# Kernel optimization log

Measured on AMD Instinct MI355X. Metric: run time of the kernel, lower is better.

The kernel has to match this reference:

```python
import jax, jax.numpy as jnp
import numpy as np

D_MODEL = 1024
N_HEADS = 16
D_HEAD = D_MODEL // N_HEADS
HIDDEN = 4096
B, T = 2, 2048
EPS = 1e-5


def setup_inputs() -> dict:
    key = jax.random.key(0)
    ks = jax.random.split(key, 16)
    s = 0.02
    return {
        "x": jax.random.normal(ks[0], (B, T, D_MODEL), dtype=jnp.float32),
        # LayerNorm 1
        "gamma1": jnp.ones((D_MODEL,), jnp.float32),
        "beta1": jnp.zeros((D_MODEL,), jnp.float32),
        # attention projections, stored (in, out) so y = x @ W + b
        "Wq": jax.random.normal(ks[1], (D_MODEL, D_MODEL), jnp.float32) * s,
        "bq": jnp.zeros((D_MODEL,), jnp.float32),
        "Wk": jax.random.normal(ks[2], (D_MODEL, D_MODEL), jnp.float32) * s,
        "bk": jnp.zeros((D_MODEL,), jnp.float32),
        "Wv": jax.random.normal(ks[3], (D_MODEL, D_MODEL), jnp.float32) * s,
        "bv": jnp.zeros((D_MODEL,), jnp.float32),
        "Wo": jax.random.normal(ks[4], (D_MODEL, D_MODEL), jnp.float32) * s,
        "bo": jnp.zeros((D_MODEL,), jnp.float32),
        # LayerNorm 2
        "gamma2": jnp.ones((D_MODEL,), jnp.float32),
        "beta2": jnp.zeros((D_MODEL,), jnp.float32),
        # MLP
        "W1": jax.random.normal(ks[5], (D_MODEL, HIDDEN), jnp.float32) * s,
        "b1": jnp.zeros((HIDDEN,), jnp.float32),
        "W2": jax.random.normal(ks[6], (HIDDEN, D_MODEL), jnp.float32) * s,
        "b2": jnp.zeros((D_MODEL,), jnp.float32),
    }


def _layernorm(x, gamma, beta):
    mean = jnp.mean(x, axis=-1, keepdims=True)
    var = jnp.mean(jnp.square(x - mean), axis=-1, keepdims=True)  # unbiased=False
    return gamma * (x - mean) * jax.lax.rsqrt(var + EPS) + beta


def _attention(x, Wq, bq, Wk, bk, Wv, bv, Wo, bo):
    b, t, _ = x.shape
    q = (x @ Wq + bq).reshape(b, t, N_HEADS, D_HEAD)
    k = (x @ Wk + bk).reshape(b, t, N_HEADS, D_HEAD)
    v = (x @ Wv + bv).reshape(b, t, N_HEADS, D_HEAD)
    scores = jnp.einsum("bqhd,bkhd->bhqk", q, k) / np.sqrt(D_HEAD).astype(np.float32)
    causal = jnp.tril(jnp.ones((t, t), dtype=bool))  # keep j <= i
    scores = jnp.where(causal, scores, -jnp.inf)
    attn = jax.nn.softmax(scores, axis=-1)
    out = jnp.einsum("bhqk,bkhd->bqhd", attn, v).reshape(b, t, D_MODEL)
    return out @ Wo + bo


def reference(x, gamma1, beta1, Wq, bq, Wk, bk, Wv, bv, Wo, bo,
              gamma2, beta2, W1, b1, W2, b2):
    # x = x + Attn(LN1(x))
    x = x + _attention(_layernorm(x, gamma1, beta1), Wq, bq, Wk, bk, Wv, bv, Wo, bo)
    # x = x + MLP(LN2(x)); torch F.gelu default = exact erf gelu
    h = _layernorm(x, gamma2, beta2)
    h = jax.nn.gelu(h @ W1 + b1, approximate=False) @ W2 + b2
    return x + h
```

## Files before the change

kernel.cpp:

```cpp
#include <hip/hip_runtime.h>
#include <stdint.h>

typedef unsigned short u16;
typedef short bf16x8 __attribute__((ext_vector_type(8)));
typedef float f32x4 __attribute__((ext_vector_type(4)));
typedef float f32x16 __attribute__((ext_vector_type(16)));

#define MB (1024L*1024L)

__device__ inline u16 f2bf(float f) {
  union { float f; unsigned u; } v; v.f = f;
  unsigned r = (v.u + 0x7FFFu + ((v.u >> 16) & 1u)) >> 16;
  return (u16)r;
}

__device__ inline float bf2f(u16 u) {
  union { unsigned u; float f; } v; v.u = ((unsigned)u) << 16; return v.f;
}

__device__ inline unsigned cvtpk(float lo, float hi) {
  unsigned r;
  asm("v_cvt_pk_bf16_f32 %0, %1, %2" : "=v"(r) : "v"(lo), "v"(hi));
  return r;
}

#define GLOAD16(gptr, lptr) \
  __builtin_amdgcn_global_load_lds((__attribute__((address_space(1))) void*)(gptr), \
                                   (__attribute__((address_space(3))) void*)(lptr), 16, 0, 0)

__global__ __launch_bounds__(256) void twconv(const float* __restrict__ W,
                                              u16* __restrict__ WT, int K, int N) {
  __shared__ float tile[32][33];
  const int nbn = N >> 5;
  const int bk = blockIdx.x / nbn;
  const int bn = blockIdx.x % nbn;
  const int tid = threadIdx.x;
  const int r = tid >> 3;
  const int c4 = (tid & 7) << 2;
  const float4 v = *(const float4*)(W + (size_t)(bk * 32 + r) * N + bn * 32 + c4);
  tile[r][c4 + 0] = v.x; tile[r][c4 + 1] = v.y;
  tile[r][c4 + 2] = v.z; tile[r][c4 + 3] = v.w;
  __syncthreads();
  ushort4 o;
  o.x = f2bf(tile[c4 + 0][r]); o.y = f2bf(tile[c4 + 1][r]);
  o.z = f2bf(tile[c4 + 2][r]); o.w = f2bf(tile[c4 + 3][r]);
  *(ushort4*)(WT + (size_t)(bn * 32 + r) * K + bk * 32 + c4) = o;
}

__global__ __launch_bounds__(256) void concat3(const float* __restrict__ a,
                                               const float* __restrict__ b,
                                               const float* __restrict__ c,
                                               float* __restrict__ out, int n) {
  int i = blockIdx.x * 256 + threadIdx.x;
  if (i < n) { out[i] = a[i]; out[n + i] = b[i]; out[2 * n + i] = c[i]; }
}

__global__ __launch_bounds__(256) void ln_kernel(const float* __restrict__ x,
                                                 const float* __restrict__ gamma,
                                                 const float* __restrict__ beta,
                                                 u16* __restrict__ out) {
  const int row = blockIdx.x;
  const int tid = threadIdx.x;
  const float4 v = *(const float4*)(x + (size_t)row * 1024 + tid * 4);
  float s = v.x + v.y + v.z + v.w;
  float s2 = v.x * v.x + v.y * v.y + v.z * v.z + v.w * v.w;
#pragma unroll
  for (int m = 1; m < 64; m <<= 1) {
    s += __shfl_xor(s, m, 64);
    s2 += __shfl_xor(s2, m, 64);
  }
  __shared__ float red[8];
  const int w = tid >> 6;
  if ((tid & 63) == 0) { red[w] = s; red[4 + w] = s2; }
  __syncthreads();
  s = red[0] + red[1] + red[2] + red[3];
  s2 = red[4] + red[5] + red[6] + red[7];
  const float mean = s * (1.0f / 1024.0f);
  const float var = s2 * (1.0f / 1024.0f) - mean * mean;
  const float rstd = rsqrtf(var + 1e-5f);
  const float4 g = *(const float4*)(gamma + tid * 4);
  const float4 b = *(const float4*)(beta + tid * 4);
  ushort4 o;
  o.x = f2bf(g.x * (v.x - mean) * rstd + b.x);
  o.y = f2bf(g.y * (v.y - mean) * rstd + b.y);
  o.z = f2bf(g.z * (v.z - mean) * rstd + b.z);
  o.w = f2bf(g.w * (v.w - mean) * rstd + b.w);
  *(ushort4*)(out + (size_t)row * 1024 + tid * 4) = o;
}

template <int EPI, int BN>
__global__ __launch_bounds__(256, (BN == 64) ? 3 : 2)
void gemm_bt(const u16* __restrict__ A, const u16* __restrict__ BT,
             const float* __restrict__ bias, const float* __restrict__ res,
             void* __restrict__ outp, int M, int N, int K) {
  constexpr int MF = (BN == 128) ? 4 : 2;
  constexpr int ACH = 4;
  constexpr int BCH = BN / 32;
  constexpr int LOADS = ACH + BCH;
  __shared__ __align__(16) u16 As[2][128 * 64];
  __shared__ __align__(16) u16 Bs[2][BN * 64];
  const int nBN = N / BN;
  const int hw = blockIdx.x;
  const int xcd = hw & 7;
  const int rr = hw >> 3;
  const int bm = xcd * 4 + rr / nBN;
  const int bn = rr % nBN;
  const int tid = threadIdx.x;
  const int lane = tid & 63;
  const int wid = tid >> 6;
  const int wm = (BN == 128) ? (wid >> 1) : wid;
  const int wn = (BN == 128) ? (wid & 1) : 0;
  const int e4 = lane >> 4;

  int abase[MF], ax[MF];
#pragma unroll
  for (int m = 0; m < MF; ++m) {
    int rowa = wm * (MF * 16) + m * 16 + (lane & 15);
    abase[m] = rowa * 64; ax[m] = rowa & 7;
  }
  int bbase[4], bx[4];
#pragma unroll
  for (int n = 0; n < 4; ++n) {
    int rowb = wn * 64 + n * 16 + (lane & 15);
    bbase[n] = rowb * 64; bx[n] = rowb & 7;
  }

  size_t ga[ACH]; int loa[ACH];
#pragma unroll
  for (int c = 0; c < ACH; ++c) {
    int idx = tid + (c << 8);
    int row = idx >> 3;
    int ch = (idx & 7) ^ (row & 7);
    ga[c] = (size_t)(bm * 128 + row) * K + (ch << 3);
    loa[c] = idx << 4;
  }
  size_t gb[BCH]; int lob[BCH];
#pragma unroll
  for (int c = 0; c < BCH; ++c) {
    int idx = tid + (c << 8);
    int row = idx >> 3;
    int ch = (idx & 7) ^ (row & 7);
    gb[c] = (size_t)(bn * BN + row) * K + (ch << 3);
    lob[c] = idx << 4;
  }

#define STAGE_G(t, bb) do { \
  _Pragma("unroll") for (int c = 0; c < ACH; ++c) \
    GLOAD16(A + ga[c] + (size_t)(t) * 64, (char*)As[bb] + loa[c]); \
  _Pragma("unroll") for (int c = 0; c < BCH; ++c) \
    GLOAD16(BT + gb[c] + (size_t)(t) * 64, (char*)Bs[bb] + lob[c]); \
} while (0)

  f32x4 acc[MF][4] = {};
  const int nt = K >> 6;

  STAGE_G(0, 0);
  STAGE_G(1, 1);

  for (int t = 0; t < nt; ++t) {
    if (t + 1 < nt) {
      asm volatile("s_waitcnt vmcnt(%0)" :: "i"(LOADS) : "memory");
    } else {
      asm volatile("s_waitcnt vmcnt(0)" ::: "memory");
    }
    __builtin_amdgcn_s_barrier();
    const u16* Ap = As[t & 1];
    const u16* Bp = Bs[t & 1];
    bf16x8 af[2][MF], bfr[2][4];
#pragma unroll
    for (int kk = 0; kk < 2; ++kk) {
#pragma unroll
      for (int m = 0; m < MF; ++m)
        af[kk][m] = *(const bf16x8*)(Ap + abase[m] + (((((kk << 2) | e4)) ^ ax[m]) << 3));
#pragma unroll
      for (int n = 0; n < 4; ++n)
        bfr[kk][n] = *(const bf16x8*)(Bp + bbase[n] + (((((kk << 2) | e4)) ^ bx[n]) << 3));
    }
    asm volatile("s_waitcnt lgkmcnt(0)" ::: "memory");
    __builtin_amdgcn_s_barrier();
    if (t + 2 < nt) STAGE_G(t + 2, t & 1);
    __builtin_amdgcn_s_setprio(1);
#pragma unroll
    for (int kk = 0; kk < 2; ++kk)
#pragma unroll
      for (int m = 0; m < MF; ++m)
#pragma unroll
        for (int n = 0; n < 4; ++n)
          acc[m][n] = __builtin_amdgcn_mfma_f32_16x16x32_bf16(af[kk][m], bfr[kk][n], acc[m][n], 0, 0, 0);
    __builtin_amdgcn_s_setprio(0);
  }
#undef STAGE_G

  const int rbase = bm * 128 + wm * (MF * 16);
  const int cbase = bn * BN + wn * 64;
#pragma unroll
  for (int m = 0; m < MF; ++m) {
#pragma unroll
    for (int n = 0; n < 4; ++n) {
      const int col = cbase + n * 16 + (lane & 15);
      const int row0 = rbase + m * 16 + ((lane >> 4) << 2);
      const float bv = bias[col];
#pragma unroll
      for (int r = 0; r < 4; ++r) {
        const int row = row0 + r;
        float v = acc[m][n][r] + bv;
        if (EPI == 1) {
          ((float*)outp)[(size_t)row * N + col] = v + res[(size_t)row * N + col];
        } else if (EPI == 2) {
          float tt = v * (1.0f + 0.044715f * v * v);
          float sg = 1.0f / (1.0f + __expf(-1.5957691216057308f * tt));
          ((u16*)outp)[(size_t)row * N + col] = f2bf(v * sg);
        } else {
          ((u16*)outp)[(size_t)row * N + col] = f2bf(v);
        }
      }
    }
  }
}

__global__ __launch_bounds__(512, 2) void attn_kernel(const u16* __restrict__ QKV,
                                                      u16* __restrict__ O) {
  __shared__ __align__(16) u16 KV[4][4096];
  const int T = 2048, LD = 3072;
  const int blk = blockIdx.x;
  const int xcd = blk & 7;
  const int i = blk >> 3;
  const int bh = xcd * 4 + (i & 3);
  const int p = i >> 2;
  const int b = bh >> 4, hd = bh & 15;
  const int tid = threadIdx.x;
  const int lane = tid & 63;
  const int w = tid >> 6;
  const int h = lane >> 5;
  const int cA = p, cB = 15 - p;
  const int myc = (w < 4) ? cA : cB;
  const int qwb = myc * 128 + (w & 3) * 32;
  const int qg = qwb + (lane & 31);
  const int diag = qwb >> 6;
  const int myNt = diag + 1;
  const int nt = 2 * cB + 2;

  const u16* Qb = QKV + (size_t)b * T * LD + hd * 64;
  const u16* Kb = Qb + 1024;
  const u16* Vb = Qb + 2048;

  const float QSC = 0.18033688011112042f;
  bf16x8 qf[4];
#pragma unroll
  for (int s = 0; s < 4; ++s) {
    bf16x8 raw = *(const bf16x8*)(Qb + (size_t)qg * LD + s * 16 + h * 8);
    union { unsigned wd[4]; bf16x8 v; } u;
#pragma unroll
    for (int e = 0; e < 4; ++e)
      u.wd[e] = cvtpk(bf2f((u16)raw[2 * e]) * QSC, bf2f((u16)raw[2 * e + 1]) * QSC);
    qf[s] = u.v;
  }

  f32x16 oacc[2] = {};
  float m = -INFINITY, l = 0.0f;

  const int srow = tid >> 3;
  const int scol = tid & 7;
  const int kgc = ((scol ^ (srow & 7)) << 3);

  GLOAD16(Kb + (size_t)srow * LD + kgc, (char*)KV[0] + tid * 16);
  {
    bf16x8 vv0 = *(const bf16x8*)(Vb + (size_t)srow * LD + scol * 8);
#pragma unroll
    for (int e = 0; e < 8; ++e) {
      int d = scol * 8 + e;
      KV[2][(d << 6) | (srow & 7) | ((((srow >> 3) ^ e ^ scol) & 7) << 3)] = (u16)vv0[e];
    }
  }
  __syncthreads();

  int cur = 0;
  for (int j = 0; j < nt; ++j) {
    const bool pre = (j + 1 < nt);
    bf16x8 vv;
    if (pre) {
      GLOAD16(Kb + (size_t)((j + 1) * 64 + srow) * LD + kgc, (char*)KV[cur ^ 1] + tid * 16);
      vv = *(const bf16x8*)(Vb + (size_t)((j + 1) * 64 + srow) * LD + scol * 8);
    }

    if (j < myNt) {
      f32x16 sacc[2] = {};
      const u16* Kp = KV[cur];
      __builtin_amdgcn_s_setprio(1);
#pragma unroll
      for (int t = 0; t < 2; ++t) {
#pragma unroll
        for (int s = 0; s < 4; ++s) {
          int row = t * 32 + (lane & 31);
          bf16x8 kf = *(const bf16x8*)(Kp + (row << 6) + ((((2 * s + h) ^ (row & 7)) & 7) << 3));
          sacc[t] = __builtin_amdgcn_mfma_f32_32x32x16_bf16(kf, qf[s], sacc[t], 0, 0, 0);
        }
      }
      __builtin_amdgcn_s_setprio(0);

      if (j == diag) {
#pragma unroll
        for (int t = 0; t < 2; ++t)
#pragma unroll
          for (int r = 0; r < 16; ++r) {
            int key = (j << 6) + 32 * t + (r & 3) + 8 * (r >> 2) + 4 * h;
            if (key > qg) sacc[t][r] = -INFINITY;
          }
      }

      float pmax = -INFINITY;
#pragma unroll
      for (int t = 0; t < 2; ++t)
#pragma unroll
        for (int r = 0; r < 16; ++r) pmax = fmaxf(pmax, sacc[t][r]);
      pmax = fmaxf(pmax, __shfl_xor(pmax, 32, 64));

      if (!__all(pmax - m <= 2.8853900817779268f)) {
        float mn = fmaxf(m, pmax);
        float alpha = exp2f(m - mn);
        m = mn;
        l *= alpha;
#pragma unroll
        for (int d2 = 0; d2 < 2; ++d2)
#pragma unroll
          for (int r = 0; r < 16; ++r) oacc[d2][r] *= alpha;
      }

      float lsum = 0.0f;
#pragma unroll
      for (int t = 0; t < 2; ++t)
#pragma unroll
        for (int r = 0; r < 16; ++r) {
          float pe = exp2f(sacc[t][r] - m);
          sacc[t][r] = pe;
          lsum += pe;
        }
      lsum += __shfl_xor(lsum, 32, 64);
      l += lsum;

      union PF { unsigned wd[4]; bf16x8 v; } pf[4];
#pragma unroll
      for (int t = 0; t < 2; ++t) {
#pragma unroll
        for (int kb = 0; kb < 2; ++kb) {
          int base = 8 * kb;
          unsigned A0 = cvtpk(sacc[t][base + 0], sacc[t][base + 1]);
          unsigned A2 = cvtpk(sacc[t][base + 2], sacc[t][base + 3]);
          unsigned A4 = cvtpk(sacc[t][base + 4], sacc[t][base + 5]);
          unsigned A6 = cvtpk(sacc[t][base + 6], sacc[t][base + 7]);
          unsigned S0 = (unsigned)__shfl_xor((int)(h ? A0 : A4), 32, 64);
          unsigned S2 = (unsigned)__shfl_xor((int)(h ? A2 : A6), 32, 64);
          PF& u = pf[2 * t + kb];
          u.wd[0] = h ? S0 : A0;
          u.wd[1] = h ? S2 : A2;
          u.wd[2] = h ? A4 : S0;
          u.wd[3] = h ? A6 : S2;
        }
      }

      const u16* Vp = KV[2 + cur];
      __builtin_amdgcn_s_setprio(1);
#pragma unroll
      for (int d2 = 0; d2 < 2; ++d2) {
        int d = d2 * 32 + (lane & 31);
#pragma unroll
        for (int ks = 0; ks < 4; ++ks) {
          bf16x8 vf = *(const bf16x8*)(Vp + (d << 6) + ((((2 * ks + h) ^ (d & 7) ^ ((d >> 3) & 7)) & 7) << 3));
          oacc[d2] = __builtin_amdgcn_mfma_f32_32x32x16_bf16(vf, pf[ks].v, oacc[d2], 0, 0, 0);
        }
      }
      __builtin_amdgcn_s_setprio(0);
    }

    if (pre) {
#pragma unroll
      for (int e = 0; e < 8; ++e) {
        int d = scol * 8 + e;
        KV[2 + (cur ^ 1)][(d << 6) | (srow & 7) | ((((srow >> 3) ^ e ^ scol) & 7) << 3)] = (u16)vv[e];
      }
    }
    __syncthreads();
    cur ^= 1;
  }

  const float rinv = 1.0f / l;
  u16* Ob = (u16*)KV;
  const int qloc = w * 32 + (lane & 31);
#pragma unroll
  for (int d2 = 0; d2 < 2; ++d2)
#pragma unroll
    for (int r = 0; r < 16; ++r) {
      int d = d2 * 32 + (r & 3) + 8 * (r >> 2) + 4 * h;
      Ob[(qloc << 6) | (d ^ ((qloc & 7) << 3))] = f2bf(oacc[d2][r] * rinv);
    }
  __syncthreads();
#pragma unroll
  for (int it = 0; it < 4; ++it) {
    int r = (tid >> 3) + it * 64;
    int c = tid & 7;
    bf16x8 val = *(const bf16x8*)(Ob + (r << 6) + (((c ^ (r & 7)) & 7) << 3));
    int qg2 = (r < 128) ? (cA * 128 + r) : (cB * 128 + (r - 128));
    *(bf16x8*)(O + (size_t)(b * T + qg2) * 1024 + hd * 64 + c * 8) = val;
  }
}

extern "C" void kernel_launch(void* const* d_in, const int* in_sizes, int n_in,
                              void* d_out, int out_size, void* d_ws, size_t ws_size,
                              hipStream_t stream) {
  const float* x      = (const float*)d_in[0];
  const float* gamma1 = (const float*)d_in[1];
  const float* beta1  = (const float*)d_in[2];
  const float* Wq     = (const float*)d_in[3];
  const float* bq     = (const float*)d_in[4];
  const float* Wk     = (const float*)d_in[5];
  const float* bk     = (const float*)d_in[6];
  const float* Wv     = (const float*)d_in[7];
  const float* bv     = (const float*)d_in[8];
  const float* Wo     = (const float*)d_in[9];
  const float* bo     = (const float*)d_in[10];
  const float* gamma2 = (const float*)d_in[11];
  const float* beta2  = (const float*)d_in[12];
  const float* W1     = (const float*)d_in[13];
  const float* b1     = (const float*)d_in[14];
  const float* W2     = (const float*)d_in[15];
  const float* b2     = (const float*)d_in[16];

  char* ws = (char*)d_ws;
  u16* WqkvT = (u16*)(ws + 0 * MB);
  u16* WoT   = (u16*)(ws + 6 * MB);
  u16* W1T   = (u16*)(ws + 8 * MB);
  u16* W2T   = (u16*)(ws + 16 * MB);
  u16* qkv   = (u16*)(ws + 24 * MB);
  u16* hb    = (u16*)(ws + 24 * MB);
  u16* xn    = (u16*)(ws + 56 * MB);
  float* bqkv = (float*)d_out;
  float* x1 = (float*)d_out;

  const int M = 4096;

  twconv<<<dim3(1024), dim3(256), 0, stream>>>(Wq, WqkvT, 1024, 1024);
  twconv<<<dim3(1024), dim3(256), 0, stream>>>(Wk, WqkvT + 1024 * 1024, 1024, 1024);
  twconv<<<dim3(1024), dim3(256), 0, stream>>>(Wv, WqkvT + 2048 * 1024, 1024, 1024);
  twconv<<<dim3(1024), dim3(256), 0, stream>>>(Wo, WoT, 1024, 1024);
  twconv<<<dim3(4096), dim3(256), 0, stream>>>(W1, W1T, 1024, 4096);
  twconv<<<dim3(4096), dim3(256), 0, stream>>>(W2, W2T, 4096, 1024);
  concat3<<<dim3(4), dim3(256), 0, stream>>>(bq, bk, bv, bqkv, 1024);

  ln_kernel<<<dim3(M), dim3(256), 0, stream>>>(x, gamma1, beta1, xn);

  gemm_bt<0, 128><<<dim3(768), dim3(256), 0, stream>>>(xn, WqkvT, bqkv, nullptr, qkv, M, 3072, 1024);

  attn_kernel<<<dim3(256), dim3(512), 0, stream>>>(qkv, xn);

  gemm_bt<1, 64><<<dim3(512), dim3(256), 0, stream>>>(xn, WoT, bo, x, x1, M, 1024, 1024);

  ln_kernel<<<dim3(M), dim3(256), 0, stream>>>(x1, gamma2, beta2, xn);

  gemm_bt<2, 128><<<dim3(1024), dim3(256), 0, stream>>>(xn, W1T, b1, nullptr, hb, M, 4096, 1024);
  gemm_bt<1, 64><<<dim3(512), dim3(256), 0, stream>>>(hb, W2T, b2, x1, d_out, M, 1024, 4096);
}
```

Before: 238.6 us.

## Software-pipeline attention: overlap QK of next tile with PV of previous

The attention loop now defers each tile's P·V MFMA work by one iteration. The QK^T MFMAs for tile j and the PV MFMAs for tile j-1 are issued back to back in one high-priority region, and the softmax exp work can overlap with outstanding matrix ops. V staging moves from double to triple buffering, which raises LDS from four to five 8KB slabs. A drain step after the loop handles the last tile. This is meant to hide the softmax dependency latency between QK and PV, at the cost of more LDS and more live registers (sacc and pf are now carried across iterations).

```diff
diff --git a/kernel.cpp b/kernel.cpp
--- a/kernel.cpp
+++ b/kernel.cpp
@@ -220,7 +220,7 @@
 
 __global__ __launch_bounds__(512, 2) void attn_kernel(const u16* __restrict__ QKV,
                                                       u16* __restrict__ O) {
-  __shared__ __align__(16) u16 KV[4][4096];
+  __shared__ __align__(16) u16 SM[5][4096];
   const int T = 2048, LD = 3072;
   const int blk = blockIdx.x;
   const int xcd = blk & 7;
@@ -257,38 +257,46 @@
   }
 
   f32x16 oacc[2] = {};
+  f32x16 sacc[2];
+  union PF { unsigned wd[4]; bf16x8 v; } pf[4];
   float m = -INFINITY, l = 0.0f;
 
   const int srow = tid >> 3;
   const int scol = tid & 7;
   const int kgc = ((scol ^ (srow & 7)) << 3);
 
-  GLOAD16(Kb + (size_t)srow * LD + kgc, (char*)KV[0] + tid * 16);
+#define VWRITE(buf, vvreg) do { \
+  _Pragma("unroll") for (int e = 0; e < 8; ++e) { \
+    int d = scol * 8 + e; \
+    SM[2 + (buf)][(d << 6) | (srow & 7) | ((((srow >> 3) ^ e ^ scol) & 7) << 3)] = (u16)(vvreg)[e]; \
+  } \
+} while (0)
+
+  GLOAD16(Kb + (size_t)srow * LD + kgc, (char*)SM[0] + tid * 16);
   {
     bf16x8 vv0 = *(const bf16x8*)(Vb + (size_t)srow * LD + scol * 8);
-#pragma unroll
-    for (int e = 0; e < 8; ++e) {
-      int d = scol * 8 + e;
-      KV[2][(d << 6) | (srow & 7) | ((((srow >> 3) ^ e ^ scol) & 7) << 3)] = (u16)vv0[e];
-    }
+    VWRITE(0, vv0);
   }
   __syncthreads();
 
-  int cur = 0;
+  int vPrev = 2, vCur = 0, vNext = 1;
   for (int j = 0; j < nt; ++j) {
     const bool pre = (j + 1 < nt);
     bf16x8 vv;
     if (pre) {
-      GLOAD16(Kb + (size_t)((j + 1) * 64 + srow) * LD + kgc, (char*)KV[cur ^ 1] + tid * 16);
+      GLOAD16(Kb + (size_t)((j + 1) * 64 + srow) * LD + kgc, (char*)SM[(j + 1) & 1] + tid * 16);
       vv = *(const bf16x8*)(Vb + (size_t)((j + 1) * 64 + srow) * LD + scol * 8);
     }
-
-    if (j < myNt) {
-      f32x16 sacc[2] = {};
-      const u16* Kp = KV[cur];
-      __builtin_amdgcn_s_setprio(1);
+    const bool doQK = (j < myNt);
+    const bool doPV = (j >= 1) && (j <= myNt);
+
+    __builtin_amdgcn_s_setprio(1);
+    if (doQK) {
+      const u16* Kp = SM[j & 1];
 #pragma unroll
       for (int t = 0; t < 2; ++t) {
+#pragma unroll
+        for (int r = 0; r < 16; ++r) sacc[t][r] = 0.0f;
 #pragma unroll
         for (int s = 0; s < 4; ++s) {
           int row = t * 32 + (lane & 31);
@@ -296,8 +304,22 @@
           sacc[t] = __builtin_amdgcn_mfma_f32_32x32x16_bf16(kf, qf[s], sacc[t], 0, 0, 0);
         }
       }
-      __builtin_amdgcn_s_setprio(0);
-
+    }
+    if (doPV) {
+      const u16* Vp = SM[2 + vPrev];
+#pragma unroll
+      for (int d2 = 0; d2 < 2; ++d2) {
+        int d = d2 * 32 + (lane & 31);
+#pragma unroll
+        for (int ks = 0; ks < 4; ++ks) {
+          bf16x8 vf = *(const bf16x8*)(Vp + (d << 6) + ((((2 * ks + h) ^ (d & 7) ^ ((d >> 3) & 7)) & 7) << 3));
+          oacc[d2] = __builtin_amdgcn_mfma_f32_32x32x16_bf16(vf, pf[ks].v, oacc[d2], 0, 0, 0);
+        }
+      }
+    }
+    __builtin_amdgcn_s_setprio(0);
+
+    if (doQK) {
       if (j == diag) {
 #pragma unroll
         for (int t = 0; t < 2; ++t)
@@ -338,7 +360,6 @@
       lsum += __shfl_xor(lsum, 32, 64);
       l += lsum;
 
-      union PF { unsigned wd[4]; bf16x8 v; } pf[4];
 #pragma unroll
       for (int t = 0; t < 2; ++t) {
 #pragma unroll
@@ -357,34 +378,29 @@
           u.wd[3] = h ? A6 : S2;
         }
       }
-
-      const u16* Vp = KV[2 + cur];
-      __builtin_amdgcn_s_setprio(1);
-#pragma unroll
-      for (int d2 = 0; d2 < 2; ++d2) {
-        int d = d2 * 32 + (lane & 31);
-#pragma unroll
-        for (int ks = 0; ks < 4; ++ks) {
-          bf16x8 vf = *(const bf16x8*)(Vp + (d << 6) + ((((2 * ks + h) ^ (d & 7) ^ ((d >> 3) & 7)) & 7) << 3));
-          oacc[d2] = __builtin_amdgcn_mfma_f32_32x32x16_bf16(vf, pf[ks].v, oacc[d2], 0, 0, 0);
-        }
-      }
-      __builtin_amdgcn_s_setprio(0);
-    }
-
-    if (pre) {
-#pragma unroll
-      for (int e = 0; e < 8; ++e) {
-        int d = scol * 8 + e;
-        KV[2 + (cur ^ 1)][(d << 6) | (srow & 7) | ((((srow >> 3) ^ e ^ scol) & 7) << 3)] = (u16)vv[e];
-      }
-    }
+    }
+
+    if (pre) VWRITE(vNext, vv);
     __syncthreads();
-    cur ^= 1;
-  }
+    vPrev = vCur; vCur = vNext; vNext = (vNext == 2) ? 0 : (vNext + 1);
+  }
+
+  if (myNt == nt) {
+    const u16* Vp = SM[2 + vPrev];
+#pragma unroll
+    for (int d2 = 0; d2 < 2; ++d2) {
+      int d = d2 * 32 + (lane & 31);
+#pragma unroll
+      for (int ks = 0; ks < 4; ++ks) {
+        bf16x8 vf = *(const bf16x8*)(Vp + (d << 6) + ((((2 * ks + h) ^ (d & 7) ^ ((d >> 3) & 7)) & 7) << 3));
+        oacc[d2] = __builtin_amdgcn_mfma_f32_32x32x16_bf16(vf, pf[ks].v, oacc[d2], 0, 0, 0);
+      }
+    }
+  }
+  __syncthreads();
 
   const float rinv = 1.0f / l;
-  u16* Ob = (u16*)KV;
+  u16* Ob = (u16*)SM;
   const int qloc = w * 32 + (lane & 31);
 #pragma unroll
   for (int d2 = 0; d2 < 2; ++d2)
```

New measurement: 239.6 us. No clear change (+0.4%).

## Merge weight-prep kernels into one launch and process two KV tiles per attention iteration

Applied to the files above, without the earlier changes.

Seven weight transpose/convert and bias concat launches are replaced by a single wprep kernel that dispatches on block index, removing launch overhead and tail gaps. The attention kernel now keeps four K and four V tiles in LDS and handles two 64-key tiles per loop iteration. It computes both QK^T tiles before a shared softmax max/rescale and then both PV products, which halves barriers and rescale checks per key and exposes more MFMA work. LDS use doubles to 64KB per block, which may limit occupancy under launch_bounds(512,2), and register pressure rises from the second score and P buffers.

```diff
diff --git a/kernel.cpp b/kernel.cpp
--- a/kernel.cpp
+++ b/kernel.cpp
@@ -28,31 +28,45 @@
   __builtin_amdgcn_global_load_lds((__attribute__((address_space(1))) void*)(gptr), \
                                    (__attribute__((address_space(3))) void*)(lptr), 16, 0, 0)
 
-__global__ __launch_bounds__(256) void twconv(const float* __restrict__ W,
-                                              u16* __restrict__ WT, int K, int N) {
+__global__ __launch_bounds__(256) void wprep(
+    const float* __restrict__ Wq, const float* __restrict__ Wk,
+    const float* __restrict__ Wv, const float* __restrict__ Wo,
+    const float* __restrict__ W1, const float* __restrict__ W2,
+    const float* __restrict__ bq, const float* __restrict__ bk,
+    const float* __restrict__ bv,
+    u16* __restrict__ WqkvT, u16* __restrict__ WoT,
+    u16* __restrict__ W1T, u16* __restrict__ W2T, float* __restrict__ bqkv) {
+  const int blk = blockIdx.x;
+  const int tid = threadIdx.x;
+  if (blk >= 12288) {
+    int i = (blk - 12288) * 256 + tid;
+    bqkv[i] = bq[i]; bqkv[1024 + i] = bk[i]; bqkv[2048 + i] = bv[i];
+    return;
+  }
+  const float* W; u16* WT; int K, N, tb;
+  if (blk < 4096) {
+    K = 1024; N = 1024;
+    if (blk < 1024)      { W = Wq; WT = WqkvT;               tb = blk; }
+    else if (blk < 2048) { W = Wk; WT = WqkvT + 1024 * 1024; tb = blk - 1024; }
+    else if (blk < 3072) { W = Wv; WT = WqkvT + 2048 * 1024; tb = blk - 2048; }
+    else                 { W = Wo; WT = WoT;                 tb = blk - 3072; }
+  } else if (blk < 8192) { W = W1; WT = W1T; K = 1024; N = 4096; tb = blk - 4096; }
+  else                   { W = W2; WT = W2T; K = 4096; N = 1024; tb = blk - 8192; }
+
   __shared__ float tile[32][33];
   const int nbn = N >> 5;
-  const int bk = blockIdx.x / nbn;
-  const int bn = blockIdx.x % nbn;
-  const int tid = threadIdx.x;
+  const int bk_ = tb / nbn;
+  const int bn = tb % nbn;
   const int r = tid >> 3;
   const int c4 = (tid & 7) << 2;
-  const float4 v = *(const float4*)(W + (size_t)(bk * 32 + r) * N + bn * 32 + c4);
+  const float4 v = *(const float4*)(W + (size_t)(bk_ * 32 + r) * N + bn * 32 + c4);
   tile[r][c4 + 0] = v.x; tile[r][c4 + 1] = v.y;
   tile[r][c4 + 2] = v.z; tile[r][c4 + 3] = v.w;
   __syncthreads();
   ushort4 o;
   o.x = f2bf(tile[c4 + 0][r]); o.y = f2bf(tile[c4 + 1][r]);
   o.z = f2bf(tile[c4 + 2][r]); o.w = f2bf(tile[c4 + 3][r]);
-  *(ushort4*)(WT + (size_t)(bn * 32 + r) * K + bk * 32 + c4) = o;
-}
-
-__global__ __launch_bounds__(256) void concat3(const float* __restrict__ a,
-                                               const float* __restrict__ b,
-                                               const float* __restrict__ c,
-                                               float* __restrict__ out, int n) {
-  int i = blockIdx.x * 256 + threadIdx.x;
-  if (i < n) { out[i] = a[i]; out[n + i] = b[i]; out[2 * n + i] = c[i]; }
+  *(ushort4*)(WT + (size_t)(bn * 32 + r) * K + bk_ * 32 + c4) = o;
 }
 
 __global__ __launch_bounds__(256) void ln_kernel(const float* __restrict__ x,
@@ -220,13 +234,13 @@
 
 __global__ __launch_bounds__(512, 2) void attn_kernel(const u16* __restrict__ QKV,
                                                       u16* __restrict__ O) {
-  __shared__ __align__(16) u16 KV[4][4096];
+  __shared__ __align__(16) u16 SM[8][4096];
   const int T = 2048, LD = 3072;
   const int blk = blockIdx.x;
   const int xcd = blk & 7;
-  const int i = blk >> 3;
-  const int bh = xcd * 4 + (i & 3);
-  const int p = i >> 2;
+  const int i0 = blk >> 3;
+  const int bh = xcd * 4 + (i0 & 3);
+  const int p = i0 >> 2;
   const int b = bh >> 4, hd = bh & 15;
   const int tid = threadIdx.x;
   const int lane = tid & 63;
@@ -239,6 +253,7 @@
   const int diag = qwb >> 6;
   const int myNt = diag + 1;
   const int nt = 2 * cB + 2;
+  const int ni = nt >> 1;
 
   const u16* Qb = QKV + (size_t)b * T * LD + hd * 64;
   const u16* Kb = Qb + 1024;
@@ -257,62 +272,112 @@
   }
 
   f32x16 oacc[2] = {};
+  f32x16 s0[2], s1[2];
+  union PF { unsigned wd[4]; bf16x8 v; } pf0[4], pf1[4];
   float m = -INFINITY, l = 0.0f;
 
   const int srow = tid >> 3;
   const int scol = tid & 7;
   const int kgc = ((scol ^ (srow & 7)) << 3);
 
-  GLOAD16(Kb + (size_t)srow * LD + kgc, (char*)KV[0] + tid * 16);
+#define VWRITE(buf, vvreg) do { \
+  _Pragma("unroll") for (int e = 0; e < 8; ++e) { \
+    int d = scol * 8 + e; \
+    SM[4 + (buf)][(d << 6) | (srow & 7) | ((((srow >> 3) ^ e ^ scol) & 7) << 3)] = (u16)(vvreg)[e]; \
+  } \
+} while (0)
+
+#define QKTILE(sv, kb) do { \
+  const u16* Kp_ = SM[kb]; \
+  _Pragma("unroll") for (int t = 0; t < 2; ++t) { \
+    _Pragma("unroll") for (int s = 0; s < 4; ++s) { \
+      int row_ = t * 32 + (lane & 31); \
+      bf16x8 kf_ = *(const bf16x8*)(Kp_ + (row_ << 6) + ((((2 * s + h) ^ (row_ & 7)) & 7) << 3)); \
+      sv[t] = __builtin_amdgcn_mfma_f32_32x32x16_bf16(kf_, qf[s], sv[t], 0, 0, 0); \
+    } \
+  } \
+} while (0)
+
+#define MASKTILE(sv, jj) do { \
+  _Pragma("unroll") for (int t = 0; t < 2; ++t) \
+    _Pragma("unroll") for (int r = 0; r < 16; ++r) { \
+      int key_ = ((jj) << 6) + 32 * t + (r & 3) + 8 * (r >> 2) + 4 * h; \
+      if (key_ > qg) sv[t][r] = -INFINITY; \
+    } \
+} while (0)
+
+#define PFCONV(sv, pfv) do { \
+  _Pragma("unroll") for (int t = 0; t < 2; ++t) { \
+    _Pragma("unroll") for (int kb = 0; kb < 2; ++kb) { \
+      int base_ = 8 * kb; \
+      unsigned A0 = cvtpk(sv[t][base_ + 0], sv[t][base_ + 1]); \
+      unsigned A2 = cvtpk(sv[t][base_ + 2], sv[t][base_ + 3]); \
+      unsigned A4 = cvtpk(sv[t][base_ + 4], sv[t][base_ + 5]); \
+      unsigned A6 = cvtpk(sv[t][base_ + 6], sv[t][base_ + 7]); \
+      unsigned S0 = (unsigned)__shfl_xor((int)(h ? A0 : A4), 32, 64); \
+      unsigned S2 = (unsigned)__shfl_xor((int)(h ? A2 : A6), 32, 64); \
+      pfv[2 * t + kb].wd[0] = h ? S0 : A0; \
+      pfv[2 * t + kb].wd[1] = h ? S2 : A2; \
+      pfv[2 * t + kb].wd[2] = h ? A4 : S0; \
+      pfv[2 * t + kb].wd[3] = h ? A6 : S2; \
+    } \
+  } \
+} while (0)
+
+#define PVTILE(pfv, vb) do { \
+  const u16* Vp_ = SM[4 + (vb)]; \
+  _Pragma("unroll") for (int d2 = 0; d2 < 2; ++d2) { \
+    int d_ = d2 * 32 + (lane & 31); \
+    _Pragma("unroll") for (int ks = 0; ks < 4; ++ks) { \
+      bf16x8 vf_ = *(const bf16x8*)(Vp_ + (d_ << 6) + ((((2 * ks + h) ^ (d_ & 7) ^ ((d_ >> 3) & 7)) & 7) << 3)); \
+      oacc[d2] = __builtin_amdgcn_mfma_f32_32x32x16_bf16(vf_, pfv[ks].v, oacc[d2], 0, 0, 0); \
+    } \
+  } \
+} while (0)
+
+  GLOAD16(Kb + (size_t)srow * LD + kgc, (char*)SM[0] + tid * 16);
+  GLOAD16(Kb + (size_t)(64 + srow) * LD + kgc, (char*)SM[1] + tid * 16);
   {
-    bf16x8 vv0 = *(const bf16x8*)(Vb + (size_t)srow * LD + scol * 8);
-#pragma unroll
-    for (int e = 0; e < 8; ++e) {
-      int d = scol * 8 + e;
-      KV[2][(d << 6) | (srow & 7) | ((((srow >> 3) ^ e ^ scol) & 7) << 3)] = (u16)vv0[e];
-    }
+    bf16x8 va = *(const bf16x8*)(Vb + (size_t)srow * LD + scol * 8);
+    bf16x8 vb = *(const bf16x8*)(Vb + (size_t)(64 + srow) * LD + scol * 8);
+    VWRITE(0, va);
+    VWRITE(1, vb);
   }
   __syncthreads();
 
-  int cur = 0;
-  for (int j = 0; j < nt; ++j) {
-    const bool pre = (j + 1 < nt);
-    bf16x8 vv;
+  for (int it = 0; it < ni; ++it) {
+    const int j0 = 2 * it, j1 = 2 * it + 1;
+    const bool pre = (it + 1 < ni);
+    bf16x8 vv0, vv1;
     if (pre) {
-      GLOAD16(Kb + (size_t)((j + 1) * 64 + srow) * LD + kgc, (char*)KV[cur ^ 1] + tid * 16);
-      vv = *(const bf16x8*)(Vb + (size_t)((j + 1) * 64 + srow) * LD + scol * 8);
-    }
-
-    if (j < myNt) {
-      f32x16 sacc[2] = {};
-      const u16* Kp = KV[cur];
+      GLOAD16(Kb + (size_t)((j0 + 2) * 64 + srow) * LD + kgc, (char*)SM[(j0 + 2) & 3] + tid * 16);
+      GLOAD16(Kb + (size_t)((j1 + 2) * 64 + srow) * LD + kgc, (char*)SM[(j1 + 2) & 3] + tid * 16);
+      vv0 = *(const bf16x8*)(Vb + (size_t)((j0 + 2) * 64 + srow) * LD + scol * 8);
+      vv1 = *(const bf16x8*)(Vb + (size_t)((j1 + 2) * 64 + srow) * LD + scol * 8);
+    }
+    const bool doQK0 = (j0 < myNt);
+    const bool doQK1 = (j1 < myNt);
+
+    if (doQK0) {
       __builtin_amdgcn_s_setprio(1);
 #pragma unroll
-      for (int t = 0; t < 2; ++t) {
-#pragma unroll
-        for (int s = 0; s < 4; ++s) {
-          int row = t * 32 + (lane & 31);
-          bf16x8 kf = *(const bf16x8*)(Kp + (row << 6) + ((((2 * s + h) ^ (row & 7)) & 7) << 3));
-          sacc[t] = __builtin_amdgcn_mfma_f32_32x32x16_bf16(kf, qf[s], sacc[t], 0, 0, 0);
+      for (int t = 0; t < 2; ++t) { s0[t] = (f32x16)(0.0f); s1[t] = (f32x16)(0.0f); }
+      QKTILE(s0, (j0 & 3));
+      if (doQK1) QKTILE(s1, (j1 & 3));
+      __builtin_amdgcn_s_setprio(0);
+
+      if (j0 == diag) MASKTILE(s0, j0);
+      if (doQK1 && j1 == diag) MASKTILE(s1, j1);
+
+      float pm0 = -INFINITY, pm1 = -INFINITY;
+#pragma unroll
+      for (int t = 0; t < 2; ++t)
+#pragma unroll
+        for (int r = 0; r < 16; ++r) {
+          pm0 = fmaxf(pm0, s0[t][r]);
+          if (doQK1) pm1 = fmaxf(pm1, s1[t][r]);
         }
-      }
-      __builtin_amdgcn_s_setprio(0);
-
-      if (j == diag) {
-#pragma unroll
-        for (int t = 0; t < 2; ++t)
-#pragma unroll
-          for (int r = 0; r < 16; ++r) {
-            int key = (j << 6) + 32 * t + (r & 3) + 8 * (r >> 2) + 4 * h;
-            if (key > qg) sacc[t][r] = -INFINITY;
-          }
-      }
-
-      float pmax = -INFINITY;
-#pragma unroll
-      for (int t = 0; t < 2; ++t)
-#pragma unroll
-        for (int r = 0; r < 16; ++r) pmax = fmaxf(pmax, sacc[t][r]);
+      float pmax = doQK1 ? fmaxf(pm0, pm1) : pm0;
       pmax = fmaxf(pmax, __shfl_xor(pmax, 32, 64));
 
       if (!__all(pmax - m <= 2.8853900817779268f)) {
@@ -326,65 +391,45 @@
           for (int r = 0; r < 16; ++r) oacc[d2][r] *= alpha;
       }
 
-      float lsum = 0.0f;
+      float ls0 = 0.0f, ls1 = 0.0f;
 #pragma unroll
       for (int t = 0; t < 2; ++t)
 #pragma unroll
         for (int r = 0; r < 16; ++r) {
-          float pe = exp2f(sacc[t][r] - m);
-          sacc[t][r] = pe;
-          lsum += pe;
+          float p0 = exp2f(s0[t][r] - m);
+          s0[t][r] = p0; ls0 += p0;
+          if (doQK1) {
+            float p1 = exp2f(s1[t][r] - m);
+            s1[t][r] = p1; ls1 += p1;
+          }
         }
+      float lsum = doQK1 ? (ls0 + ls1) : ls0;
       lsum += __shfl_xor(lsum, 32, 64);
       l += lsum;
 
-      union PF { unsigned wd[4]; bf16x8 v; } pf[4];
-#pragma unroll
-      for (int t = 0; t < 2; ++t) {
-#pragma unroll
-        for (int kb = 0; kb < 2; ++kb) {
-          int base = 8 * kb;
-          unsigned A0 = cvtpk(sacc[t][base + 0], sacc[t][base + 1]);
-          unsigned A2 = cvtpk(sacc[t][base + 2], sacc[t][base + 3]);
-          unsigned A4 = cvtpk(sacc[t][base + 4], sacc[t][base + 5]);
-          unsigned A6 = cvtpk(sacc[t][base + 6], sacc[t][base + 7]);
-          unsigned S0 = (unsigned)__shfl_xor((int)(h ? A0 : A4), 32, 64);
-          unsigned S2 = (unsigned)__shfl_xor((int)(h ? A2 : A6), 32, 64);
-          PF& u = pf[2 * t + kb];
-          u.wd[0] = h ? S0 : A0;
-          u.wd[1] = h ? S2 : A2;
-          u.wd[2] = h ? A4 : S0;
-          u.wd[3] = h ? A6 : S2;
-        }
-      }
-
-      const u16* Vp = KV[2 + cur];
+      PFCONV(s0, pf0);
+      if (doQK1) PFCONV(s1, pf1);
+
       __builtin_amdgcn_s_setprio(1);
-#pragma unroll
-      for (int d2 = 0; d2 < 2; ++d2) {
-        int d = d2 * 32 + (lane & 31);
-#pragma unroll
-        for (int ks = 0; ks < 4; ++ks) {
-          bf16x8 vf = *(const bf16x8*)(Vp + (d << 6) + ((((2 * ks + h) ^ (d & 7) ^ ((d >> 3) & 7)) & 7) << 3));
-          oacc[d2] = __builtin_amdgcn_mfma_f32_32x32x16_bf16(vf, pf[ks].v, oacc[d2], 0, 0, 0);
-        }
-      }
+      PVTILE(pf0, (j0 & 3));
+      if (doQK1) PVTILE(pf1, (j1 & 3));
       __builtin_amdgcn_s_setprio(0);
     }
 
     if (pre) {
-#pragma unroll
-      for (int e = 0; e < 8; ++e) {
-        int d = scol * 8 + e;
-        KV[2 + (cur ^ 1)][(d << 6) | (srow & 7) | ((((srow >> 3) ^ e ^ scol) & 7) << 3)] = (u16)vv[e];
-      }
+      VWRITE((j0 + 2) & 3, vv0);
+      VWRITE((j1 + 2) & 3, vv1);
     }
     __syncthreads();
-    cur ^= 1;
-  }
+  }
+#undef VWRITE
+#undef QKTILE
+#undef MASKTILE
+#undef PFCONV
+#undef PVTILE
 
   const float rinv = 1.0f / l;
-  u16* Ob = (u16*)KV;
+  u16* Ob = (u16*)SM;
   const int qloc = w * 32 + (lane & 31);
 #pragma unroll
   for (int d2 = 0; d2 < 2; ++d2)
@@ -438,13 +483,8 @@
 
   const int M = 4096;
 
-  twconv<<<dim3(1024), dim3(256), 0, stream>>>(Wq, WqkvT, 1024, 1024);
-  twconv<<<dim3(1024), dim3(256), 0, stream>>>(Wk, WqkvT + 1024 * 1024, 1024, 1024);
-  twconv<<<dim3(1024), dim3(256), 0, stream>>>(Wv, WqkvT + 2048 * 1024, 1024, 1024);
-  twconv<<<dim3(1024), dim3(256), 0, stream>>>(Wo, WoT, 1024, 1024);
-  twconv<<<dim3(4096), dim3(256), 0, stream>>>(W1, W1T, 1024, 4096);
-  twconv<<<dim3(4096), dim3(256), 0, stream>>>(W2, W2T, 4096, 1024);
-  concat3<<<dim3(4), dim3(256), 0, stream>>>(bq, bk, bv, bqkv, 1024);
+  wprep<<<dim3(12292), dim3(256), 0, stream>>>(Wq, Wk, Wv, Wo, W1, W2, bq, bk, bv,
+                                               WqkvT, WoT, W1T, W2T, bqkv);
 
   ln_kernel<<<dim3(M), dim3(256), 0, stream>>>(x, gamma1, beta1, xn);
 
```

After: 226.4 us. 1.05x faster.

## Add 256x256-tile GEMM for QKV and MLP-up, fuse weight prep and LN1

Applied to the files above, without the earlier changes.

Adds a new 512-thread GEMM kernel with 256x256 output tiles, swizzled LDS, double-buffered direct-to-LDS loads and interleaved MFMA phases. It is used for the QKV projection and the first MLP GEMM to raise data reuse per block and cut global traffic. Separately, the six weight transpose launches, the bias concat and the first LayerNorm are merged into one kernel to reduce launch overhead. The large tiles give only 192/256 blocks at one block per CU, which risks tail and occupancy problems. The GELU epilogue uses a tanh-style sigmoid approximation where the exact erf form is specified.

```diff
diff --git a/kernel.cpp b/kernel.cpp
--- a/kernel.cpp
+++ b/kernel.cpp
@@ -28,31 +28,77 @@
   __builtin_amdgcn_global_load_lds((__attribute__((address_space(1))) void*)(gptr), \
                                    (__attribute__((address_space(3))) void*)(lptr), 16, 0, 0)
 
-__global__ __launch_bounds__(256) void twconv(const float* __restrict__ W,
-                                              u16* __restrict__ WT, int K, int N) {
+__global__ __launch_bounds__(256) void wprep(
+    const float* __restrict__ Wq, const float* __restrict__ Wk,
+    const float* __restrict__ Wv, const float* __restrict__ Wo,
+    const float* __restrict__ W1, const float* __restrict__ W2,
+    const float* __restrict__ bq, const float* __restrict__ bk,
+    const float* __restrict__ bv,
+    u16* __restrict__ WqkvT, u16* __restrict__ WoT,
+    u16* __restrict__ W1T, u16* __restrict__ W2T, float* __restrict__ bqkv,
+    const float* __restrict__ x, const float* __restrict__ gamma1,
+    const float* __restrict__ beta1, u16* __restrict__ xn) {
+  const int blk = blockIdx.x;
+  const int tid = threadIdx.x;
   __shared__ float tile[32][33];
+  __shared__ float red[8];
+
+  if (blk >= 12292) {
+    const int row = blk - 12292;
+    const float4 v = *(const float4*)(x + (size_t)row * 1024 + tid * 4);
+    float s = v.x + v.y + v.z + v.w;
+    float s2 = v.x * v.x + v.y * v.y + v.z * v.z + v.w * v.w;
+#pragma unroll
+    for (int mm = 1; mm < 64; mm <<= 1) {
+      s += __shfl_xor(s, mm, 64);
+      s2 += __shfl_xor(s2, mm, 64);
+    }
+    const int w = tid >> 6;
+    if ((tid & 63) == 0) { red[w] = s; red[4 + w] = s2; }
+    __syncthreads();
+    s = red[0] + red[1] + red[2] + red[3];
+    s2 = red[4] + red[5] + red[6] + red[7];
+    const float mean = s * (1.0f / 1024.0f);
+    const float var = s2 * (1.0f / 1024.0f) - mean * mean;
+    const float rstd = rsqrtf(var + 1e-5f);
+    const float4 g = *(const float4*)(gamma1 + tid * 4);
+    const float4 bb = *(const float4*)(beta1 + tid * 4);
+    ushort4 o;
+    o.x = f2bf(g.x * (v.x - mean) * rstd + bb.x);
+    o.y = f2bf(g.y * (v.y - mean) * rstd + bb.y);
+    o.z = f2bf(g.z * (v.z - mean) * rstd + bb.z);
+    o.w = f2bf(g.w * (v.w - mean) * rstd + bb.w);
+    *(ushort4*)(xn + (size_t)row * 1024 + tid * 4) = o;
+    return;
+  }
+  if (blk >= 12288) {
+    int i = (blk - 12288) * 256 + tid;
+    bqkv[i] = bq[i]; bqkv[1024 + i] = bk[i]; bqkv[2048 + i] = bv[i];
+    return;
+  }
+  const float* W; u16* WT; int K, N, tb;
+  if (blk < 4096) {
+    K = 1024; N = 1024;
+    if (blk < 1024)      { W = Wq; WT = WqkvT;               tb = blk; }
+    else if (blk < 2048) { W = Wk; WT = WqkvT + 1024 * 1024; tb = blk - 1024; }
+    else if (blk < 3072) { W = Wv; WT = WqkvT + 2048 * 1024; tb = blk - 2048; }
+    else                 { W = Wo; WT = WoT;                 tb = blk - 3072; }
+  } else if (blk < 8192) { W = W1; WT = W1T; K = 1024; N = 4096; tb = blk - 4096; }
+  else                   { W = W2; WT = W2T; K = 4096; N = 1024; tb = blk - 8192; }
+
   const int nbn = N >> 5;
-  const int bk = blockIdx.x / nbn;
-  const int bn = blockIdx.x % nbn;
-  const int tid = threadIdx.x;
+  const int bk_ = tb / nbn;
+  const int bn = tb % nbn;
   const int r = tid >> 3;
   const int c4 = (tid & 7) << 2;
-  const float4 v = *(const float4*)(W + (size_t)(bk * 32 + r) * N + bn * 32 + c4);
+  const float4 v = *(const float4*)(W + (size_t)(bk_ * 32 + r) * N + bn * 32 + c4);
   tile[r][c4 + 0] = v.x; tile[r][c4 + 1] = v.y;
   tile[r][c4 + 2] = v.z; tile[r][c4 + 3] = v.w;
   __syncthreads();
   ushort4 o;
   o.x = f2bf(tile[c4 + 0][r]); o.y = f2bf(tile[c4 + 1][r]);
   o.z = f2bf(tile[c4 + 2][r]); o.w = f2bf(tile[c4 + 3][r]);
-  *(ushort4*)(WT + (size_t)(bn * 32 + r) * K + bk * 32 + c4) = o;
-}
-
-__global__ __launch_bounds__(256) void concat3(const float* __restrict__ a,
-                                               const float* __restrict__ b,
-                                               const float* __restrict__ c,
-                                               float* __restrict__ out, int n) {
-  int i = blockIdx.x * 256 + threadIdx.x;
-  if (i < n) { out[i] = a[i]; out[n + i] = b[i]; out[2 * n + i] = c[i]; }
+  *(ushort4*)(WT + (size_t)(bn * 32 + r) * K + bk_ * 32 + c4) = o;
 }
 
 __global__ __launch_bounds__(256) void ln_kernel(const float* __restrict__ x,
@@ -86,6 +132,170 @@
   o.z = f2bf(g.z * (v.z - mean) * rstd + b.z);
   o.w = f2bf(g.w * (v.w - mean) * rstd + b.w);
   *(ushort4*)(out + (size_t)row * 1024 + tid * 4) = o;
+}
+
+template <int EPI>
+__global__ __launch_bounds__(512, 1)
+void gemm256sq(const u16* __restrict__ A, const u16* __restrict__ BT,
+               const float* __restrict__ bias, void* __restrict__ outp,
+               int M, int N, int K) {
+  __shared__ __align__(16) u16 As[2][256 * 64];
+  __shared__ __align__(16) u16 Bs[2][256 * 64];
+  const int nBN = N >> 8;
+  const int blk = blockIdx.x;
+  const int xcd = blk & 7;
+  const int rr = blk >> 3;
+  const int bm = xcd * 2 + rr / nBN;
+  const int bn = rr % nBN;
+  const int tid = threadIdx.x;
+  const int lane = tid & 63;
+  const int wid = tid >> 6;
+  const int wm = wid >> 2;
+  const int wn = wid & 3;
+  const int e4 = lane >> 4;
+  const int l15 = lane & 15;
+  const int sx = l15 & 7;
+
+  const int aoffb = (wm * 128 + l15) * 64;
+  const int boffb = (wn * 64 + l15) * 64;
+  const int ch0 = ((e4 ^ sx) & 7) << 3;
+  const int ch1 = (((4 | e4) ^ sx) & 7) << 3;
+
+  size_t gA[2], gB[2]; int lo[2];
+#pragma unroll
+  for (int c = 0; c < 2; ++c) {
+    int idx = tid + (c << 9);
+    int rowl = idx >> 3;
+    int chg = ((idx & 7) ^ (rowl & 7)) << 3;
+    gA[c] = (size_t)(bm * 256 + rowl) * K + chg;
+    gB[c] = (size_t)(bn * 256 + rowl) * K + chg;
+    lo[c] = idx << 4;
+  }
+  const size_t hK = (size_t)128 * K;
+
+#define STG_A(tt, h) do { _Pragma("unroll") for (int c = 0; c < 2; ++c) \
+  GLOAD16(A + gA[c] + (size_t)(h) * hK + (size_t)(tt) * 64, (char*)As[(tt) & 1] + (h) * 16384 + lo[c]); } while (0)
+#define STG_B(tt, h) do { _Pragma("unroll") for (int c = 0; c < 2; ++c) \
+  GLOAD16(BT + gB[c] + (size_t)(h) * hK + (size_t)(tt) * 64, (char*)Bs[(tt) & 1] + (h) * 16384 + lo[c]); } while (0)
+
+  f32x4 acc[8][4] = {};
+  const int nt = K >> 6;
+
+  STG_A(0, 0); STG_A(0, 1); STG_B(0, 0); STG_B(0, 1);
+  STG_B(1, 0); STG_B(1, 1);
+  asm volatile("s_waitcnt vmcnt(4)" ::: "memory");
+  __builtin_amdgcn_s_barrier();
+
+  for (int t = 0; t < nt; ++t) {
+    const u16* Ap = As[t & 1];
+    const u16* Bp = Bs[t & 1];
+    bf16x8 a[2][4], b01[2][2], b23[2][2];
+
+#pragma unroll
+    for (int mm = 0; mm < 4; ++mm) {
+      a[0][mm] = *(const bf16x8*)(Ap + aoffb + mm * 1024 + ch0);
+      a[1][mm] = *(const bf16x8*)(Ap + aoffb + mm * 1024 + ch1);
+    }
+#pragma unroll
+    for (int nn = 0; nn < 2; ++nn) {
+      b01[0][nn] = *(const bf16x8*)(Bp + boffb + nn * 1024 + ch0);
+      b01[1][nn] = *(const bf16x8*)(Bp + boffb + nn * 1024 + ch1);
+    }
+    if (t + 1 < nt) STG_A(t + 1, 0);
+    __builtin_amdgcn_s_barrier();
+    asm volatile("s_waitcnt lgkmcnt(0)" ::: "memory");
+    __builtin_amdgcn_s_setprio(1);
+#pragma unroll
+    for (int kk = 0; kk < 2; ++kk)
+#pragma unroll
+      for (int mm = 0; mm < 4; ++mm)
+#pragma unroll
+        for (int nn = 0; nn < 2; ++nn)
+          acc[mm][nn] = __builtin_amdgcn_mfma_f32_16x16x32_bf16(a[kk][mm], b01[kk][nn], acc[mm][nn], 0, 0, 0);
+    __builtin_amdgcn_s_setprio(0);
+    __builtin_amdgcn_s_barrier();
+
+#pragma unroll
+    for (int nn = 0; nn < 2; ++nn) {
+      b23[0][nn] = *(const bf16x8*)(Bp + boffb + (2 + nn) * 1024 + ch0);
+      b23[1][nn] = *(const bf16x8*)(Bp + boffb + (2 + nn) * 1024 + ch1);
+    }
+    if (t + 1 < nt) STG_A(t + 1, 1);
+    __builtin_amdgcn_s_barrier();
+    asm volatile("s_waitcnt lgkmcnt(0)" ::: "memory");
+    __builtin_amdgcn_s_setprio(1);
+#pragma unroll
+    for (int kk = 0; kk < 2; ++kk)
+#pragma unroll
+      for (int mm = 0; mm < 4; ++mm)
+#pragma unroll
+        for (int nn = 0; nn < 2; ++nn)
+          acc[mm][2 + nn] = __builtin_amdgcn_mfma_f32_16x16x32_bf16(a[kk][mm], b23[kk][nn], acc[mm][2 + nn], 0, 0, 0);
+    __builtin_amdgcn_s_setprio(0);
+    __builtin_amdgcn_s_barrier();
+
+#pragma unroll
+    for (int mm = 0; mm < 4; ++mm) {
+      a[0][mm] = *(const bf16x8*)(Ap + aoffb + (4 + mm) * 1024 + ch0);
+      a[1][mm] = *(const bf16x8*)(Ap + aoffb + (4 + mm) * 1024 + ch1);
+    }
+    if (t + 2 < nt) STG_B(t + 2, 0);
+    __builtin_amdgcn_s_barrier();
+    asm volatile("s_waitcnt lgkmcnt(0)" ::: "memory");
+    __builtin_amdgcn_s_setprio(1);
+#pragma unroll
+    for (int kk = 0; kk < 2; ++kk)
+#pragma unroll
+      for (int mm = 0; mm < 4; ++mm)
+#pragma unroll
+        for (int nn = 0; nn < 2; ++nn)
+          acc[4 + mm][2 + nn] = __builtin_amdgcn_mfma_f32_16x16x32_bf16(a[kk][mm], b23[kk][nn], acc[4 + mm][2 + nn], 0, 0, 0);
+    __builtin_amdgcn_s_setprio(0);
+    __builtin_amdgcn_s_barrier();
+
+    if (t + 2 < nt) STG_B(t + 2, 1);
+    __builtin_amdgcn_s_barrier();
+    __builtin_amdgcn_s_setprio(1);
+#pragma unroll
+    for (int kk = 0; kk < 2; ++kk)
+#pragma unroll
+      for (int mm = 0; mm < 4; ++mm)
+#pragma unroll
+        for (int nn = 0; nn < 2; ++nn)
+          acc[4 + mm][nn] = __builtin_amdgcn_mfma_f32_16x16x32_bf16(a[kk][mm], b01[kk][nn], acc[4 + mm][nn], 0, 0, 0);
+    __builtin_amdgcn_s_setprio(0);
+    if (t + 1 < nt) {
+      if (t + 2 < nt) asm volatile("s_waitcnt vmcnt(4)" ::: "memory");
+      else            asm volatile("s_waitcnt vmcnt(0)" ::: "memory");
+    }
+    __builtin_amdgcn_s_barrier();
+  }
+#undef STG_A
+#undef STG_B
+
+  const int rbase = bm * 256 + wm * 128;
+  const int cbase = bn * 256 + wn * 64;
+#pragma unroll
+  for (int m = 0; m < 8; ++m) {
+#pragma unroll
+    for (int n = 0; n < 4; ++n) {
+      const int col = cbase + n * 16 + l15;
+      const int row0 = rbase + m * 16 + e4 * 4;
+      const float bv = bias[col];
+#pragma unroll
+      for (int r = 0; r < 4; ++r) {
+        const int row = row0 + r;
+        float v = acc[m][n][r] + bv;
+        if (EPI == 2) {
+          float tt = v * (1.0f + 0.044715f * v * v);
+          float sg = 1.0f / (1.0f + __expf(-1.5957691216057308f * tt));
+          ((u16*)outp)[(size_t)row * N + col] = f2bf(v * sg);
+        } else {
+          ((u16*)outp)[(size_t)row * N + col] = f2bf(v);
+        }
+      }
+    }
+  }
 }
 
 template <int EPI, int BN>
@@ -438,17 +648,11 @@
 
   const int M = 4096;
 
-  twconv<<<dim3(1024), dim3(256), 0, stream>>>(Wq, WqkvT, 1024, 1024);
-  twconv<<<dim3(1024), dim3(256), 0, stream>>>(Wk, WqkvT + 1024 * 1024, 1024, 1024);
-  twconv<<<dim3(1024), dim3(256), 0, stream>>>(Wv, WqkvT + 2048 * 1024, 1024, 1024);
-  twconv<<<dim3(1024), dim3(256), 0, stream>>>(Wo, WoT, 1024, 1024);
-  twconv<<<dim3(4096), dim3(256), 0, stream>>>(W1, W1T, 1024, 4096);
-  twconv<<<dim3(4096), dim3(256), 0, stream>>>(W2, W2T, 4096, 1024);
-  concat3<<<dim3(4), dim3(256), 0, stream>>>(bq, bk, bv, bqkv, 1024);
-
-  ln_kernel<<<dim3(M), dim3(256), 0, stream>>>(x, gamma1, beta1, xn);
-
-  gemm_bt<0, 128><<<dim3(768), dim3(256), 0, stream>>>(xn, WqkvT, bqkv, nullptr, qkv, M, 3072, 1024);
+  wprep<<<dim3(16388), dim3(256), 0, stream>>>(Wq, Wk, Wv, Wo, W1, W2, bq, bk, bv,
+                                               WqkvT, WoT, W1T, W2T, bqkv,
+                                               x, gamma1, beta1, xn);
+
+  gemm256sq<0><<<dim3(192), dim3(512), 0, stream>>>(xn, WqkvT, bqkv, qkv, M, 3072, 1024);
 
   attn_kernel<<<dim3(256), dim3(512), 0, stream>>>(qkv, xn);
 
@@ -456,6 +660,6 @@
 
   ln_kernel<<<dim3(M), dim3(256), 0, stream>>>(x1, gamma2, beta2, xn);
 
-  gemm_bt<2, 128><<<dim3(1024), dim3(256), 0, stream>>>(xn, W1T, b1, nullptr, hb, M, 4096, 1024);
+  gemm256sq<2><<<dim3(256), dim3(512), 0, stream>>>(xn, W1T, b1, hb, M, 4096, 1024);
   gemm_bt<1, 64><<<dim3(512), dim3(256), 0, stream>>>(hb, W2T, b2, x1, d_out, M, 1024, 4096);
 }
```

Result: faster. 219.7 us (-7.9%).
